# Optimization experiments

Measured on AMD Instinct MI355X. Metric: run time of the kernel, lower is better.

## Reference

```python
import jax, jax.numpy as jnp
import numpy as np

B, L, N, C = 2, 12, 2048, 3
H, ND, TE, KS, KT = 64, 32, 10, 2, 3
BN_EPS = 1e-5


def setup_inputs() -> dict:
    key = jax.random.key(0)
    ks = jax.random.split(key, 20)
    return {
        "history_data": jax.random.normal(ks[0], (B, L, N, C), jnp.float32),
        "node_embedding_d": jax.random.normal(ks[1], (N, ND), jnp.float32),
        "node_embedding_u": jax.random.normal(ks[2], (N, ND), jnp.float32),
        "time_in_day_feat": jax.random.normal(ks[3], (B, L, N, TE), jnp.float32),
        "day_in_week_feat": jax.random.normal(ks[4], (B, L, N, TE), jnp.float32),
        "adj_mask_0": jax.random.uniform(ks[5], (N, N), jnp.float32),
        "adj_mask_1": jax.random.uniform(ks[6], (N, N), jnp.float32),
        "W1": jax.random.normal(ks[7], (2 * H, L), jnp.float32) * 0.1,
        "b1": jax.random.normal(ks[8], (2 * H,), jnp.float32) * 0.1,
        "bn_gamma": jax.random.uniform(ks[9], (2 * H,), jnp.float32) + 0.5,
        "bn_beta": jax.random.normal(ks[10], (2 * H,), jnp.float32) * 0.1,
        "bn_mean": jax.random.normal(ks[11], (2 * H,), jnp.float32) * 0.1,
        "bn_var": jax.random.uniform(ks[12], (2 * H,), jnp.float32) + 0.5,
        "W2": jax.random.normal(ks[13], (H, 2 * H), jnp.float32) * 0.1,
        "b2": jax.random.normal(ks[14], (H,), jnp.float32) * 0.1,
        "WQ": jax.random.normal(ks[15], (H, H + ND + 2 * TE), jnp.float32) * 0.1,
        "WK": jax.random.normal(ks[16], (H, H + ND + 2 * TE), jnp.float32) * 0.1,
    }


def reference(history_data, node_embedding_d, node_embedding_u,
              time_in_day_feat, day_in_week_feat, adj_mask_0, adj_mask_1,
              W1, b1, bn_gamma, bn_beta, bn_mean, bn_var, W2, b2, WQ, WK):
    b = history_data.shape[0]
    n = history_data.shape[2]

    # --- DistanceFunction (eval mode: dropout=identity, BN uses running stats) ---
    X = jnp.transpose(history_data[..., 0], (0, 2, 1))          # [B, N, L]
    h = jax.nn.relu(jnp.einsum('bnl,hl->bnh', X, W1) + b1)      # [B, N, 2H]
    h = (h - bn_mean) * jax.lax.rsqrt(bn_var + BN_EPS) * bn_gamma + bn_beta
    dy_feat = jnp.einsum('bnk,hk->bnh', h, W2) + b2             # [B, N, H]

    T_D = time_in_day_feat[:, -1]                               # [B, N, TE]
    D_W = day_in_week_feat[:, -1]                               # [B, N, TE]
    emb1 = jnp.broadcast_to(node_embedding_d[None], (b, n, node_embedding_d.shape[-1]))
    emb2 = jnp.broadcast_to(node_embedding_u[None], (b, n, node_embedding_u.shape[-1]))

    scale = 1.0 / np.sqrt(H).astype(np.float32)

    def attn_adj(feat):
        Q = jnp.einsum('bnf,hf->bnh', feat, WQ)
        K = jnp.einsum('bnf,hf->bnh', feat, WK)
        scores = jnp.einsum('bnh,bmh->bnm', Q, K) * scale       # [B, N, N]
        return jax.nn.softmax(scores, axis=-1)

    A1 = attn_adj(jnp.concatenate([dy_feat, T_D, D_W, emb1], axis=-1))
    A2 = attn_adj(jnp.concatenate([dy_feat, T_D, D_W, emb2], axis=-1))

    # --- Mask ---
    A1 = (adj_mask_0 + 1e-7)[None] * A1
    A2 = (adj_mask_1 + 1e-7)[None] * A2

    # --- Normalizer: diag_embed(1/deg) @ A  == row-scaling ---
    def norm(A):
        inv = 1.0 / jnp.sum(A, axis=2)                          # [B, N]
        inv = jnp.where(jnp.isfinite(inv), inv, 0.0)
        return inv[..., None] * A

    A1, A2 = norm(A1), norm(A2)

    # --- MultiOrder (order=KS): zero the diagonal of each k-hop graph ---
    offdiag = 1.0 - jnp.eye(n, dtype=A1.dtype)

    def multi_order(g):
        out = [g * offdiag]
        k = g
        for _ in range(2, KS + 1):
            k = jnp.matmul(k, g)
            out.append(k * offdiag)
        return out

    ordered = multi_order(A1) + multi_order(A2)

    # --- st_localization: [B,N,N] -> [B,N,KT*N] via repeat along a new axis ---
    def localize(g):
        g = jnp.broadcast_to(g[:, :, None, :], (b, n, KT, n))
        return g.reshape(b, n, KT * n)

    return tuple(localize(g) for g in ordered)
```

## Files before the change

kernel.cpp:

```cpp
#include <hip/hip_runtime.h>
#include <cstdint>

typedef unsigned short u16;

#define NB 2
#define NL 12
#define NN_ 2048
#define NH 64
#define NF 116
constexpr size_t NSQ = (size_t)NN_ * NN_;
constexpr size_t OUT_PER = (size_t)NB * NN_ * 3 * NN_;

__device__ __forceinline__ u16 f2bf(float f) {
    union { float f; unsigned u; } v; v.f = f;
    unsigned r = 0x7FFFu + ((v.u >> 16) & 1u);
    return (u16)((v.u + r) >> 16);
}

__global__ __launch_bounds__(128) void feat_kernel(
    const float* __restrict__ hist, const float* __restrict__ embd, const float* __restrict__ embu,
    const float* __restrict__ tid, const float* __restrict__ diw,
    const float* __restrict__ W1, const float* __restrict__ b1,
    const float* __restrict__ gamma, const float* __restrict__ beta,
    const float* __restrict__ mean, const float* __restrict__ var,
    const float* __restrict__ W2, const float* __restrict__ b2,
    const float* __restrict__ WQ, const float* __restrict__ WK,
    float* __restrict__ qk) {
    int bn = blockIdx.x;
    int b = bn >> 11, n = bn & (NN_ - 1);
    __shared__ float X[NL];
    __shared__ float hsh[128];
    __shared__ float feat[84];
    int t = threadIdx.x;
    if (t < NL) X[t] = hist[((size_t)(b * NL + t) * NN_ + n) * 3];
    __syncthreads();
    float acc = b1[t];
#pragma unroll
    for (int l = 0; l < NL; ++l) acc += X[l] * W1[t * NL + l];
    acc = fmaxf(acc, 0.f);
    acc = (acc - mean[t]) * rsqrtf(var[t] + 1e-5f) * gamma[t] + beta[t];
    hsh[t] = acc;
    __syncthreads();
    if (t < 64) {
        float d = b2[t];
#pragma unroll 8
        for (int j = 0; j < 128; ++j) d += hsh[j] * W2[t * 128 + j];
        feat[t] = d;
    } else {
        int u = t - 64;
        if (u < 10) feat[64 + u] = tid[((size_t)(b * NL + (NL - 1)) * NN_ + n) * 10 + u];
        else if (u < 20) feat[64 + u] = diw[((size_t)(b * NL + (NL - 1)) * NN_ + n) * 10 + (u - 10)];
    }
    __syncthreads();
    const float* W = (t < 64) ? WQ : WK;
    int row = t & 63;
    float s = 0.f;
    for (int f = 0; f < 84; ++f) s += feat[f] * W[row * NF + f];
    float s1 = s, s2 = s;
    for (int u2 = 0; u2 < 32; ++u2) {
        float w = W[row * NF + 84 + u2];
        s1 += w * embd[n * 32 + u2];
        s2 += w * embu[n * 32 + u2];
    }
    int qsel = (t < 64) ? 0 : 1;
    const size_t MS = (size_t)NB * NN_ * NH;
    size_t base = ((size_t)b * NN_ + n) * NH + row;
    qk[(size_t)(0 * 2 + qsel) * MS + base] = s1;
    qk[(size_t)(1 * 2 + qsel) * MS + base] = s2;
}

__device__ __forceinline__ void score_tile(const float (*Qs)[68], const float (*Ks)[68],
                                           int rq, int cu, float s[4][4]) {
#pragma unroll
    for (int i = 0; i < 4; ++i)
#pragma unroll
        for (int j = 0; j < 4; ++j) s[i][j] = 0.f;
#pragma unroll
    for (int k = 0; k < 64; k += 4) {
        float4 qv[4], kv[4];
#pragma unroll
        for (int i = 0; i < 4; ++i) qv[i] = *(const float4*)&Qs[rq * 4 + i][k];
#pragma unroll
        for (int j = 0; j < 4; ++j) kv[j] = *(const float4*)&Ks[j * 32 + cu][k];
#pragma unroll
        for (int i = 0; i < 4; ++i)
#pragma unroll
            for (int j = 0; j < 4; ++j)
                s[i][j] += qv[i].x * kv[j].x + qv[i].y * kv[j].y + qv[i].z * kv[j].z + qv[i].w * kv[j].w;
    }
}

__global__ __launch_bounds__(256) void attn_kernel(const float* __restrict__ qk,
                                                   const float* __restrict__ mask0,
                                                   const float* __restrict__ mask1,
                                                   u16* __restrict__ G,
                                                   float* __restrict__ out) {
    int a = blockIdx.z, b = blockIdx.y, tile = blockIdx.x;
    int mat = a * 2 + b;
    const float* mask = a ? mask1 : mask0;
    const size_t MS = (size_t)NB * NN_ * NH;
    const float* Q = qk + (size_t)(a * 2 + 0) * MS + (size_t)b * NN_ * NH;
    const float* K = qk + (size_t)(a * 2 + 1) * MS + (size_t)b * NN_ * NH;
    __shared__ float Qs[32][68];
    __shared__ float Ks[128][68];
    __shared__ float redm[32][33];
    __shared__ float redsum[32][33];
    __shared__ float rowM[32], rowInv[32];
    int t = threadIdx.x;
    int rq = t >> 5, cu = t & 31;
    {
        const float4* Qsrc = (const float4*)(Q + (size_t)tile * 32 * NH);
        for (int i = t; i < 32 * 16; i += 256)
            *(float4*)&Qs[i >> 4][(i & 15) * 4] = Qsrc[i];
    }
    float mx[4], sm[4];
#pragma unroll
    for (int i = 0; i < 4; ++i) { mx[i] = -1e30f; sm[i] = 0.f; }
    for (int c = 0; c < NN_ / 128; ++c) {
        __syncthreads();
        const float4* Ksrc = (const float4*)(K + (size_t)c * 128 * NH);
        for (int i = t; i < 128 * 16; i += 256)
            *(float4*)&Ks[i >> 4][(i & 15) * 4] = Ksrc[i];
        __syncthreads();
        float s[4][4];
        score_tile(Qs, Ks, rq, cu, s);
#pragma unroll
        for (int i = 0; i < 4; ++i) {
            int nrow = tile * 32 + rq * 4 + i;
#pragma unroll
            for (int j = 0; j < 4; ++j) {
                int m = c * 128 + j * 32 + cu;
                float sc = s[i][j] * 0.125f;
                float w = mask[(size_t)nrow * NN_ + m] + 1e-7f;
                if (sc > mx[i]) { sm[i] *= __expf(mx[i] - sc); mx[i] = sc; }
                sm[i] += w * __expf(sc - mx[i]);
            }
        }
    }
#pragma unroll
    for (int i = 0; i < 4; ++i) { redm[rq * 4 + i][cu] = mx[i]; redsum[rq * 4 + i][cu] = sm[i]; }
    __syncthreads();
    if (t < 32) {
        float M = -1e30f;
        for (int c2 = 0; c2 < 32; ++c2) M = fmaxf(M, redm[t][c2]);
        float S = 0.f;
        for (int c2 = 0; c2 < 32; ++c2) S += redsum[t][c2] * __expf(redm[t][c2] - M);
        rowM[t] = M;
        rowInv[t] = 1.f / S;
    }
    __syncthreads();
    for (int c = 0; c < NN_ / 128; ++c) {
        __syncthreads();
        const float4* Ksrc = (const float4*)(K + (size_t)c * 128 * NH);
        for (int i = t; i < 128 * 16; i += 256)
            *(float4*)&Ks[i >> 4][(i & 15) * 4] = Ksrc[i];
        __syncthreads();
        float s[4][4];
        score_tile(Qs, Ks, rq, cu, s);
#pragma unroll
        for (int i = 0; i < 4; ++i) {
            int nrow = tile * 32 + rq * 4 + i;
            float M = rowM[rq * 4 + i], inv = rowInv[rq * 4 + i];
            size_t ob = (size_t)(2 * a) * OUT_PER + ((size_t)b * NN_ + nrow) * (size_t)(3 * NN_);
#pragma unroll
            for (int j = 0; j < 4; ++j) {
                int m = c * 128 + j * 32 + cu;
                float sc = s[i][j] * 0.125f;
                float w = mask[(size_t)nrow * NN_ + m] + 1e-7f;
                float val = w * __expf(sc - M) * inv;
                G[(size_t)mat * NSQ + (size_t)nrow * NN_ + m] = f2bf(val);
                float ov = (m == nrow) ? 0.f : val;
                out[ob + m] = ov;
                out[ob + NN_ + m] = ov;
                out[ob + 2 * NN_ + m] = ov;
            }
        }
    }
}

__global__ __launch_bounds__(256) void transpose_kernel(const u16* __restrict__ G,
                                                        u16* __restrict__ GT) {
    __shared__ u16 tl[64][72];
    int t = threadIdx.x;
    int mat = blockIdx.z;
    int c0 = blockIdx.x * 64, r0 = blockIdx.y * 64;
    const u16* Gm = G + (size_t)mat * NSQ;
    u16* GTm = GT + (size_t)mat * NSQ;
#pragma unroll
    for (int i = 0; i < 2; ++i) {
        int v = t + 256 * i, row = v >> 3, seg = v & 7;
        *(uint4*)&tl[row][seg * 8] = *(const uint4*)&Gm[(size_t)(r0 + row) * NN_ + c0 + seg * 8];
    }
    __syncthreads();
#pragma unroll
    for (int i = 0; i < 2; ++i) {
        int v = t + 256 * i, cc = v >> 3, seg = v & 7;
        union { u16 h[8]; uint4 u; } tmp;
#pragma unroll
        for (int q = 0; q < 8; ++q) tmp.h[q] = tl[seg * 8 + q][cc];
        *(uint4*)&GTm[(size_t)(c0 + cc) * NN_ + r0 + seg * 8] = tmp.u;
    }
}

typedef __attribute__((ext_vector_type(8))) short bf8v;
typedef __attribute__((ext_vector_type(4))) float f4v;

__global__ __launch_bounds__(256) void matmul_kernel(const u16* __restrict__ G,
                                                     const u16* __restrict__ GT,
                                                     float* __restrict__ out) {
    __shared__ __align__(16) char smraw[64 * 132 * 4];
    u16* smab = (u16*)smraw;
    float* smc = (float*)smraw;
    int t = threadIdx.x;
    int mat = blockIdx.z;
    int a = mat >> 1, b = mat & 1;
    int m0 = blockIdx.y * 128, n0 = blockIdx.x * 128;
    const u16* Gm = G + (size_t)mat * NSQ;
    const u16* GTm = GT + (size_t)mat * NSQ;
    int lane = t & 63, wv = t >> 6, wm = wv >> 1, wn = wv & 1;
    int m16 = lane & 15, quad = lane >> 4;
    f4v acc[4][4];
#pragma unroll
    for (int i = 0; i < 4; ++i)
#pragma unroll
        for (int j = 0; j < 4; ++j)
#pragma unroll
            for (int r = 0; r < 4; ++r) acc[i][j][r] = 0.f;

    for (int k0 = 0; k0 < NN_; k0 += 64) {
#pragma unroll
        for (int i = 0; i < 4; ++i) {
            int v = t + 256 * i, row = v >> 3, seg = v & 7;
            *(uint4*)&smab[row * 64 + seg * 8] =
                *(const uint4*)&Gm[(size_t)(m0 + row) * NN_ + k0 + seg * 8];
            *(uint4*)&smab[8192 + row * 64 + seg * 8] =
                *(const uint4*)&GTm[(size_t)(n0 + row) * NN_ + k0 + seg * 8];
        }
        __syncthreads();
#pragma unroll
        for (int kk = 0; kk < 64; kk += 32) {
            bf8v af[4], bfr[4];
#pragma unroll
            for (int i = 0; i < 4; ++i)
                af[i] = *(const bf8v*)&smab[(wm * 64 + i * 16 + m16) * 64 + kk + quad * 8];
#pragma unroll
            for (int j = 0; j < 4; ++j)
                bfr[j] = *(const bf8v*)&smab[8192 + (wn * 64 + j * 16 + m16) * 64 + kk + quad * 8];
#pragma unroll
            for (int i = 0; i < 4; ++i)
#pragma unroll
                for (int j = 0; j < 4; ++j)
                    acc[i][j] = __builtin_amdgcn_mfma_f32_16x16x32_bf16(af[i], bfr[j], acc[i][j], 0, 0, 0);
        }
        __syncthreads();
    }
#pragma unroll
    for (int p = 0; p < 2; ++p) {
        __syncthreads();
        if (wm == p) {
#pragma unroll
            for (int i = 0; i < 4; ++i)
#pragma unroll
                for (int j = 0; j < 4; ++j)
#pragma unroll
                    for (int r = 0; r < 4; ++r)
                        smc[(i * 16 + quad * 4 + r) * 132 + wn * 64 + j * 16 + m16] = acc[i][j][r];
        }
        __syncthreads();
        size_t ob0 = (size_t)(2 * a + 1) * OUT_PER;
        for (int v = t; v < 64 * 32; v += 256) {
            int row = v >> 5, seg = v & 31;
            float4 vv = *(float4*)&smc[row * 132 + seg * 4];
            int grow = m0 + p * 64 + row;
            int gcol = n0 + seg * 4;
            if (grow >= gcol && grow < gcol + 4) ((float*)&vv)[grow - gcol] = 0.f;
            size_t ob = ob0 + ((size_t)b * NN_ + grow) * (size_t)(3 * NN_) + gcol;
            *(float4*)&out[ob] = vv;
            *(float4*)&out[ob + NN_] = vv;
            *(float4*)&out[ob + 2 * NN_] = vv;
        }
    }
}

extern "C" void kernel_launch(void* const* d_in, const int* in_sizes, int n_in,
                              void* d_out, int out_size, void* d_ws, size_t ws_size,
                              hipStream_t stream) {
    const float* hist = (const float*)d_in[0];
    const float* embd = (const float*)d_in[1];
    const float* embu = (const float*)d_in[2];
    const float* tid = (const float*)d_in[3];
    const float* diw = (const float*)d_in[4];
    const float* mask0 = (const float*)d_in[5];
    const float* mask1 = (const float*)d_in[6];
    const float* W1 = (const float*)d_in[7];
    const float* b1 = (const float*)d_in[8];
    const float* gamma = (const float*)d_in[9];
    const float* beta = (const float*)d_in[10];
    const float* mean = (const float*)d_in[11];
    const float* var = (const float*)d_in[12];
    const float* W2 = (const float*)d_in[13];
    const float* b2 = (const float*)d_in[14];
    const float* WQ = (const float*)d_in[15];
    const float* WK = (const float*)d_in[16];

    float* qk = (float*)d_ws;
    u16* G = (u16*)((char*)d_ws + (size_t)4 * 1024 * 1024);
    u16* GT = (u16*)((char*)d_ws + (size_t)4 * 1024 * 1024 + 4 * NSQ * sizeof(u16));
    float* out = (float*)d_out;

    feat_kernel<<<dim3(NB * NN_), dim3(128), 0, stream>>>(
        hist, embd, embu, tid, diw, W1, b1, gamma, beta, mean, var, W2, b2, WQ, WK, qk);
    attn_kernel<<<dim3(NN_ / 32, NB, 2), dim3(256), 0, stream>>>(qk, mask0, mask1, G, out);
    transpose_kernel<<<dim3(32, 32, 4), dim3(256), 0, stream>>>(G, GT);
    matmul_kernel<<<dim3(16, 16, 4), dim3(256), 0, stream>>>(G, GT, out);
}
```

Before: 739.9 us.

## Split attention into materialized scores and row-normalize kernels; use direct global-to-LDS loads

The fused two-pass attention kernel recomputed QK scores twice and wrote outputs with scalar stores. It is replaced by a scores kernel that writes the full fp32 score matrix to workspace and a per-row normalize kernel. The normalize kernel does the max and sum with wave shuffles and writes G and the triplicated outputs with vectorized stores. The matmul kernel also switches its tile loads to global_load_lds, which skips the register round-trip. In exchange this adds about 64MB of score traffic to and from HBM and one extra launch.

```diff
diff --git a/kernel.cpp b/kernel.cpp
--- a/kernel.cpp
+++ b/kernel.cpp
@@ -16,6 +16,11 @@
     unsigned r = 0x7FFFu + ((v.u >> 16) & 1u);
     return (u16)((v.u + r) >> 16);
 }
+
+#define GLOAD_LDS16(g, l)                                                  \
+    __builtin_amdgcn_global_load_lds(                                      \
+        (const __attribute__((address_space(1))) unsigned int*)(g),        \
+        (__attribute__((address_space(3))) unsigned int*)(l), 16, 0, 0)
 
 __global__ __launch_bounds__(128) void feat_kernel(
     const float* __restrict__ hist, const float* __restrict__ embd, const float* __restrict__ embu,
@@ -69,113 +74,111 @@
     qk[(size_t)(1 * 2 + qsel) * MS + base] = s2;
 }
 
-__device__ __forceinline__ void score_tile(const float (*Qs)[68], const float (*Ks)[68],
-                                           int rq, int cu, float s[4][4]) {
-#pragma unroll
-    for (int i = 0; i < 4; ++i)
-#pragma unroll
-        for (int j = 0; j < 4; ++j) s[i][j] = 0.f;
-#pragma unroll
-    for (int k = 0; k < 64; k += 4) {
-        float4 qv[4], kv[4];
-#pragma unroll
-        for (int i = 0; i < 4; ++i) qv[i] = *(const float4*)&Qs[rq * 4 + i][k];
-#pragma unroll
-        for (int j = 0; j < 4; ++j) kv[j] = *(const float4*)&Ks[j * 32 + cu][k];
-#pragma unroll
-        for (int i = 0; i < 4; ++i)
-#pragma unroll
-            for (int j = 0; j < 4; ++j)
-                s[i][j] += qv[i].x * kv[j].x + qv[i].y * kv[j].y + qv[i].z * kv[j].z + qv[i].w * kv[j].w;
-    }
-}
-
-__global__ __launch_bounds__(256) void attn_kernel(const float* __restrict__ qk,
-                                                   const float* __restrict__ mask0,
-                                                   const float* __restrict__ mask1,
-                                                   u16* __restrict__ G,
-                                                   float* __restrict__ out) {
-    int a = blockIdx.z, b = blockIdx.y, tile = blockIdx.x;
-    int mat = a * 2 + b;
-    const float* mask = a ? mask1 : mask0;
+__global__ __launch_bounds__(256) void scores_kernel(const float* __restrict__ qk,
+                                                     float* __restrict__ S) {
+    int mat = blockIdx.z;
+    int a = mat >> 1, b = mat & 1;
     const size_t MS = (size_t)NB * NN_ * NH;
     const float* Q = qk + (size_t)(a * 2 + 0) * MS + (size_t)b * NN_ * NH;
     const float* K = qk + (size_t)(a * 2 + 1) * MS + (size_t)b * NN_ * NH;
-    __shared__ float Qs[32][68];
+    int n0 = blockIdx.y * 64;
+    int m0 = blockIdx.x * 128;
+    __shared__ float Qs[64][68];
     __shared__ float Ks[128][68];
-    __shared__ float redm[32][33];
-    __shared__ float redsum[32][33];
-    __shared__ float rowM[32], rowInv[32];
-    int t = threadIdx.x;
-    int rq = t >> 5, cu = t & 31;
+    int t = threadIdx.x;
     {
-        const float4* Qsrc = (const float4*)(Q + (size_t)tile * 32 * NH);
-        for (int i = t; i < 32 * 16; i += 256)
+        const float4* Qsrc = (const float4*)(Q + (size_t)n0 * NH);
+        for (int i = t; i < 64 * 16; i += 256)
             *(float4*)&Qs[i >> 4][(i & 15) * 4] = Qsrc[i];
-    }
-    float mx[4], sm[4];
-#pragma unroll
-    for (int i = 0; i < 4; ++i) { mx[i] = -1e30f; sm[i] = 0.f; }
-    for (int c = 0; c < NN_ / 128; ++c) {
-        __syncthreads();
-        const float4* Ksrc = (const float4*)(K + (size_t)c * 128 * NH);
+        const float4* Ksrc = (const float4*)(K + (size_t)m0 * NH);
         for (int i = t; i < 128 * 16; i += 256)
             *(float4*)&Ks[i >> 4][(i & 15) * 4] = Ksrc[i];
-        __syncthreads();
-        float s[4][4];
-        score_tile(Qs, Ks, rq, cu, s);
-#pragma unroll
-        for (int i = 0; i < 4; ++i) {
-            int nrow = tile * 32 + rq * 4 + i;
-#pragma unroll
-            for (int j = 0; j < 4; ++j) {
-                int m = c * 128 + j * 32 + cu;
-                float sc = s[i][j] * 0.125f;
-                float w = mask[(size_t)nrow * NN_ + m] + 1e-7f;
-                if (sc > mx[i]) { sm[i] *= __expf(mx[i] - sc); mx[i] = sc; }
-                sm[i] += w * __expf(sc - mx[i]);
-            }
-        }
-    }
-#pragma unroll
-    for (int i = 0; i < 4; ++i) { redm[rq * 4 + i][cu] = mx[i]; redsum[rq * 4 + i][cu] = sm[i]; }
-    __syncthreads();
-    if (t < 32) {
-        float M = -1e30f;
-        for (int c2 = 0; c2 < 32; ++c2) M = fmaxf(M, redm[t][c2]);
-        float S = 0.f;
-        for (int c2 = 0; c2 < 32; ++c2) S += redsum[t][c2] * __expf(redm[t][c2] - M);
-        rowM[t] = M;
-        rowInv[t] = 1.f / S;
-    }
-    __syncthreads();
-    for (int c = 0; c < NN_ / 128; ++c) {
-        __syncthreads();
-        const float4* Ksrc = (const float4*)(K + (size_t)c * 128 * NH);
-        for (int i = t; i < 128 * 16; i += 256)
-            *(float4*)&Ks[i >> 4][(i & 15) * 4] = Ksrc[i];
-        __syncthreads();
-        float s[4][4];
-        score_tile(Qs, Ks, rq, cu, s);
-#pragma unroll
-        for (int i = 0; i < 4; ++i) {
-            int nrow = tile * 32 + rq * 4 + i;
-            float M = rowM[rq * 4 + i], inv = rowInv[rq * 4 + i];
-            size_t ob = (size_t)(2 * a) * OUT_PER + ((size_t)b * NN_ + nrow) * (size_t)(3 * NN_);
-#pragma unroll
-            for (int j = 0; j < 4; ++j) {
-                int m = c * 128 + j * 32 + cu;
-                float sc = s[i][j] * 0.125f;
-                float w = mask[(size_t)nrow * NN_ + m] + 1e-7f;
-                float val = w * __expf(sc - M) * inv;
-                G[(size_t)mat * NSQ + (size_t)nrow * NN_ + m] = f2bf(val);
-                float ov = (m == nrow) ? 0.f : val;
-                out[ob + m] = ov;
-                out[ob + NN_ + m] = ov;
-                out[ob + 2 * NN_ + m] = ov;
-            }
-        }
-    }
+    }
+    __syncthreads();
+    int rq = t >> 5, cu = t & 31;
+    float acc[8][4];
+#pragma unroll
+    for (int i = 0; i < 8; ++i)
+#pragma unroll
+        for (int j = 0; j < 4; ++j) acc[i][j] = 0.f;
+#pragma unroll
+    for (int kc = 0; kc < 16; ++kc) {
+        float4 qv[8], kv[4];
+#pragma unroll
+        for (int i = 0; i < 8; ++i) qv[i] = *(const float4*)&Qs[rq * 8 + i][kc * 4];
+#pragma unroll
+        for (int j = 0; j < 4; ++j) kv[j] = *(const float4*)&Ks[j * 32 + cu][kc * 4];
+#pragma unroll
+        for (int i = 0; i < 8; ++i)
+#pragma unroll
+            for (int j = 0; j < 4; ++j)
+                acc[i][j] += qv[i].x * kv[j].x + qv[i].y * kv[j].y + qv[i].z * kv[j].z + qv[i].w * kv[j].w;
+    }
+    float* Sm = S + (size_t)mat * NSQ;
+#pragma unroll
+    for (int i = 0; i < 8; ++i) {
+        size_t rb = (size_t)(n0 + rq * 8 + i) * NN_ + m0;
+#pragma unroll
+        for (int j = 0; j < 4; ++j) Sm[rb + j * 32 + cu] = acc[i][j] * 0.125f;
+    }
+}
+
+__global__ __launch_bounds__(256) void normalize_kernel(const float* __restrict__ S,
+                                                        const float* __restrict__ mask0,
+                                                        const float* __restrict__ mask1,
+                                                        u16* __restrict__ G,
+                                                        float* __restrict__ out) {
+    int n = blockIdx.x;
+    int mat = blockIdx.y;
+    int a = mat >> 1, b = mat & 1;
+    const float* mask = a ? mask1 : mask0;
+    const float* Srow = S + ((size_t)mat * NN_ + n) * NN_;
+    const float* Mrow = mask + (size_t)n * NN_;
+    int t = threadIdx.x;
+    int c0 = t * 8;
+    float4 s0 = *(const float4*)&Srow[c0];
+    float4 s1 = *(const float4*)&Srow[c0 + 4];
+    float4 k0 = *(const float4*)&Mrow[c0];
+    float4 k1 = *(const float4*)&Mrow[c0 + 4];
+    float sv[8] = {s0.x, s0.y, s0.z, s0.w, s1.x, s1.y, s1.z, s1.w};
+    float mv[8] = {k0.x, k0.y, k0.z, k0.w, k1.x, k1.y, k1.z, k1.w};
+    float mx = sv[0];
+#pragma unroll
+    for (int i = 1; i < 8; ++i) mx = fmaxf(mx, sv[i]);
+#pragma unroll
+    for (int off = 32; off >= 1; off >>= 1) mx = fmaxf(mx, __shfl_xor(mx, off, 64));
+    __shared__ float redA[4], redB[4];
+    int wv = t >> 6;
+    if ((t & 63) == 0) redA[wv] = mx;
+    __syncthreads();
+    mx = fmaxf(fmaxf(redA[0], redA[1]), fmaxf(redA[2], redA[3]));
+    float w[8];
+    float sum = 0.f;
+#pragma unroll
+    for (int i = 0; i < 8; ++i) {
+        w[i] = (mv[i] + 1e-7f) * __expf(sv[i] - mx);
+        sum += w[i];
+    }
+#pragma unroll
+    for (int off = 32; off >= 1; off >>= 1) sum += __shfl_xor(sum, off, 64);
+    if ((t & 63) == 0) redB[wv] = sum;
+    __syncthreads();
+    float inv = 1.f / (redB[0] + redB[1] + redB[2] + redB[3]);
+    union { u16 h[8]; uint4 u; } gv;
+    float ov[8];
+#pragma unroll
+    for (int i = 0; i < 8; ++i) {
+        float val = w[i] * inv;
+        gv.h[i] = f2bf(val);
+        ov[i] = (c0 + i == n) ? 0.f : val;
+    }
+    *(uint4*)&G[((size_t)mat * NSQ + (size_t)n * NN_) + c0] = gv.u;
+    size_t ob = (size_t)(2 * a) * OUT_PER + ((size_t)b * NN_ + n) * (size_t)(3 * NN_) + c0;
+    float4 o0 = {ov[0], ov[1], ov[2], ov[3]};
+    float4 o1 = {ov[4], ov[5], ov[6], ov[7]};
+    *(float4*)&out[ob] = o0;        *(float4*)&out[ob + 4] = o1;
+    *(float4*)&out[ob + NN_] = o0;  *(float4*)&out[ob + NN_ + 4] = o1;
+    *(float4*)&out[ob + 2 * NN_] = o0; *(float4*)&out[ob + 2 * NN_ + 4] = o1;
 }
 
 __global__ __launch_bounds__(256) void transpose_kernel(const u16* __restrict__ G,
@@ -219,6 +222,7 @@
     const u16* GTm = GT + (size_t)mat * NSQ;
     int lane = t & 63, wv = t >> 6, wm = wv >> 1, wn = wv & 1;
     int m16 = lane & 15, quad = lane >> 4;
+    int lrow = lane >> 3, lseg = lane & 7;
     f4v acc[4][4];
 #pragma unroll
     for (int i = 0; i < 4; ++i)
@@ -230,11 +234,11 @@
     for (int k0 = 0; k0 < NN_; k0 += 64) {
 #pragma unroll
         for (int i = 0; i < 4; ++i) {
-            int v = t + 256 * i, row = v >> 3, seg = v & 7;
-            *(uint4*)&smab[row * 64 + seg * 8] =
-                *(const uint4*)&Gm[(size_t)(m0 + row) * NN_ + k0 + seg * 8];
-            *(uint4*)&smab[8192 + row * 64 + seg * 8] =
-                *(const uint4*)&GTm[(size_t)(n0 + row) * NN_ + k0 + seg * 8];
+            int r0 = wv * 32 + i * 8;
+            const u16* ga = Gm + (size_t)(m0 + r0 + lrow) * NN_ + k0 + lseg * 8;
+            GLOAD_LDS16(ga, &smab[r0 * 64]);
+            const u16* gb = GTm + (size_t)(n0 + r0 + lrow) * NN_ + k0 + lseg * 8;
+            GLOAD_LDS16(gb, &smab[8192 + r0 * 64]);
         }
         __syncthreads();
 #pragma unroll
@@ -303,14 +307,17 @@
     const float* WQ = (const float*)d_in[15];
     const float* WK = (const float*)d_in[16];
 
-    float* qk = (float*)d_ws;
-    u16* G = (u16*)((char*)d_ws + (size_t)4 * 1024 * 1024);
-    u16* GT = (u16*)((char*)d_ws + (size_t)4 * 1024 * 1024 + 4 * NSQ * sizeof(u16));
+    char* ws = (char*)d_ws;
+    float* qk = (float*)ws;
+    float* S  = (float*)(ws + (size_t)8 * 1024 * 1024);
+    u16* G    = (u16*)(ws + (size_t)80 * 1024 * 1024);
+    u16* GT   = (u16*)(ws + (size_t)116 * 1024 * 1024);
     float* out = (float*)d_out;
 
     feat_kernel<<<dim3(NB * NN_), dim3(128), 0, stream>>>(
         hist, embd, embu, tid, diw, W1, b1, gamma, beta, mean, var, W2, b2, WQ, WK, qk);
-    attn_kernel<<<dim3(NN_ / 32, NB, 2), dim3(256), 0, stream>>>(qk, mask0, mask1, G, out);
+    scores_kernel<<<dim3(16, 32, 4), dim3(256), 0, stream>>>(qk, S);
+    normalize_kernel<<<dim3(NN_, 4), dim3(256), 0, stream>>>(S, mask0, mask1, G, out);
     transpose_kernel<<<dim3(32, 32, 4), dim3(256), 0, stream>>>(G, GT);
     matmul_kernel<<<dim3(16, 16, 4), dim3(256), 0, stream>>>(G, GT, out);
 }
```

Result: faster. 641.1 us (-13.4%).
